# Optimization experiments

Measured on AMD Instinct MI355X. Metric: run time of the kernel, lower is better.

## Reference

```python
import jax, jax.numpy as jnp
import numpy as np

LN_EPS = 1e-5
BN_EPS = 1e-5


def setup_inputs() -> dict:
    key = jax.random.key(0)
    ks = jax.random.split(key, 16)
    b, n = 16, 256
    sc = 0.1
    inp = {
        "x": jax.random.normal(ks[0], (b, n, 4), jnp.float32),
        # proj: Linear(4, 64)
        "proj_w": jax.random.normal(ks[1], (4, 64), jnp.float32) * sc,
        "proj_b": jnp.zeros((64,), jnp.float32),
        # sigma_net: Linear(128,64) -> LayerNorm(64) -> ReLU -> Linear(64,1) -> Softplus
        "s_w1": jax.random.normal(ks[2], (128, 64), jnp.float32) * sc,
        "s_b1": jnp.zeros((64,), jnp.float32),
        "ln_g": jnp.ones((64,), jnp.float32),
        "ln_b": jnp.zeros((64,), jnp.float32),
        "s_w2": jax.random.normal(ks[3], (64, 1), jnp.float32) * sc,
        "s_b2": jnp.zeros((1,), jnp.float32),
        # gnn weight
        "gnn_w": jax.random.normal(ks[4], (64, 64), jnp.float32) * sc,
        # classifier: Linear(128,64) -> BatchNorm1d(64) -> ELU -> Dropout(eval) -> Linear(64,2)
        "c_w1": jax.random.normal(ks[5], (128, 64), jnp.float32) * sc,
        "c_b1": jnp.zeros((64,), jnp.float32),
        "bn_g": jnp.ones((64,), jnp.float32),
        "bn_b": jnp.zeros((64,), jnp.float32),
        "bn_mean": jnp.zeros((64,), jnp.float32),
        "bn_var": jnp.ones((64,), jnp.float32),
        "c_w2": jax.random.normal(ks[6], (64, 2), jnp.float32) * sc,
        "c_b2": jnp.zeros((2,), jnp.float32),
    }
    return inp


def reference(x, proj_w, proj_b, s_w1, s_b1, ln_g, ln_b, s_w2, s_b2,
              gnn_w, c_w1, c_b1, bn_g, bn_b, bn_mean, bn_var, c_w2, c_b2):
    # h: [b, n, 64]
    h = jax.nn.elu(x @ proj_w + proj_b)

    # sigma_net(cat([xi, xj])) == hi @ s_w1[:64] + hj @ s_w1[64:] + s_b1, broadcast pairwise
    a_i = h @ s_w1[:64]            # [b, n, 64]
    a_j = h @ s_w1[64:]            # [b, n, 64]
    pre = a_i[:, :, None, :] + a_j[:, None, :, :] + s_b1  # [b, n, n, 64]
    mu = jnp.mean(pre, axis=-1, keepdims=True)
    var = jnp.mean((pre - mu) ** 2, axis=-1, keepdims=True)
    ln = (pre - mu) * jax.lax.rsqrt(var + LN_EPS) * ln_g + ln_b
    sig_pre = jax.nn.relu(ln) @ s_w2 + s_b2               # [b, n, n, 1]
    sigmas = jax.nn.softplus(sig_pre[..., 0])             # [b, n, n]

    # squared pairwise distance via gram trick: ||hi - hj||^2
    sq = jnp.sum(h * h, axis=-1)                          # [b, n]
    gram = jnp.einsum("bid,bjd->bij", h, h)               # [b, n, n]
    d2 = jnp.maximum(sq[:, :, None] + sq[:, None, :] - 2.0 * gram, 0.0)
    adj = jnp.exp(-d2 / (2.0 * sigmas ** 2 + 1e-6))       # [b, n, n]

    h_agg = jnp.einsum("bij,bjd->bid", adj, h) @ gnn_w    # [b, n, 64]
    h_res = jax.nn.elu(h_agg + h)

    pooled = jnp.concatenate([h_res.mean(axis=1), h_res.max(axis=1)], axis=1)  # [b, 128]

    z = pooled @ c_w1 + c_b1
    z = (z - bn_mean) * jax.lax.rsqrt(bn_var + BN_EPS) * bn_g + bn_b  # BN eval mode
    z = jax.nn.elu(z)                                      # Dropout is identity in eval
    return z @ c_w2 + c_b2                                 # [b, 2]
```

## Files before the change

kernel.cpp:

```cpp
#include <hip/hip_runtime.h>
#include <math.h>

#define OFF_H      0
#define OFF_HT     262144
#define OFF_AI     524288
#define OFF_AJT    786432
#define OFF_SAI    1048576
#define OFF_QAI    1052672
#define OFF_SAJ    1056768
#define OFF_QAJ    1060864
#define OFF_SQH    1064960
#define OFF_HRES   1069056

__device__ __forceinline__ float elu_f(float x) { return x > 0.f ? x : expm1f(x); }

__global__ __launch_bounds__(256) void k1_embed(
    const float* __restrict__ x,
    const float* __restrict__ proj_w, const float* __restrict__ proj_b,
    const float* __restrict__ s_w1, const float* __restrict__ s_b1,
    float* __restrict__ h, float* __restrict__ hT,
    float* __restrict__ a_i, float* __restrict__ a_jT,
    float* __restrict__ sa_i, float* __restrict__ qa_i,
    float* __restrict__ sa_j, float* __restrict__ qa_j,
    float* __restrict__ sqh)
{
    __shared__ float w_sh[8192];
    int tid = threadIdx.x;
    #pragma unroll
    for (int r = 0; r < 8; ++r)
        *(float4*)&w_sh[(r*256 + tid)*4] = *(const float4*)&s_w1[(r*256 + tid)*4];
    __syncthreads();

    int lane = tid & 63;
    int wave = tid >> 6;
    int row0 = blockIdx.x * 8;

    float pw0 = proj_w[lane], pw1 = proj_w[64+lane], pw2 = proj_w[128+lane],
          pw3 = proj_w[192+lane], pb = proj_b[lane], b1 = s_b1[lane];

    #pragma unroll
    for (int r = 0; r < 2; ++r) {
        int row = row0 + wave*2 + r;
        int b = row >> 8, i = row & 255;
        float4 xv = *(const float4*)&x[row*4];
        float hv = elu_f(xv.x*pw0 + xv.y*pw1 + xv.z*pw2 + xv.w*pw3 + pb);

        float ai = b1, aj = 0.f;
        #pragma unroll 8
        for (int e = 0; e < 64; ++e) {
            float he = __shfl(hv, e);
            ai = fmaf(he, w_sh[e*64 + lane], ai);
            aj = fmaf(he, w_sh[(64+e)*64 + lane], aj);
        }
        h[row*64 + lane]   = hv;
        hT[b*64*256 + lane*256 + i] = hv;
        a_i[row*64 + lane] = ai;
        a_jT[b*64*256 + lane*256 + i] = aj;

        float v1 = ai, v2 = ai*ai, v3 = aj, v4 = aj*aj, v5 = hv*hv;
        #pragma unroll
        for (int off = 32; off > 0; off >>= 1) {
            v1 += __shfl_xor(v1, off);
            v2 += __shfl_xor(v2, off);
            v3 += __shfl_xor(v3, off);
            v4 += __shfl_xor(v4, off);
            v5 += __shfl_xor(v5, off);
        }
        if (lane == 0) {
            sa_i[row] = v1; qa_i[row] = v2;
            sa_j[row] = v3; qa_j[row] = v4;
            sqh[row]  = v5;
        }
    }
}

__global__ __launch_bounds__(256) void k2_pair(
    const float* __restrict__ a_i, const float* __restrict__ a_jT,
    const float* __restrict__ h, const float* __restrict__ hT,
    const float* __restrict__ sa_i, const float* __restrict__ qa_i,
    const float* __restrict__ sa_j, const float* __restrict__ qa_j,
    const float* __restrict__ sqh,
    const float* __restrict__ ln_g, const float* __restrict__ ln_b,
    const float* __restrict__ s_w2, const float* __restrict__ s_b2,
    const float* __restrict__ gnn_w,
    float* __restrict__ h_res)
{
    int bi0 = blockIdx.x * 4;
    int b   = bi0 >> 8;
    int j   = threadIdx.x;
    int gj  = b*256 + j;

    __shared__ float aiT[64][4], hiT[64][4];
    __shared__ float gbw[64][4];
    __shared__ float sai_s[4], qai_s[4], sqi_s[4];
    __shared__ float adj_sh[256][4];
    __shared__ float part_sh[4][4][64];
    __shared__ float hagg_sh[4][64];

    {
        int i = j >> 6, d = j & 63;
        aiT[d][i] = a_i[(bi0+i)*64 + d];
        hiT[d][i] = h[(bi0+i)*64 + d];
    }
    if (j < 64) {
        gbw[j][0] = ln_g[j]; gbw[j][1] = ln_b[j]; gbw[j][2] = s_w2[j]; gbw[j][3] = 0.f;
    }
    if (j < 4) {
        sai_s[j] = sa_i[bi0+j]; qai_s[j] = qa_i[bi0+j]; sqi_s[j] = sqh[bi0+j];
    }
    float saj = sa_j[gj], qaj = qa_j[gj], sqj = sqh[gj];
    float b2  = s_b2[0];
    __syncthreads();

    const float* ajb = a_jT + b*64*256;
    const float* htb = hT   + b*64*256;

    float ga[4] = {0.f,0.f,0.f,0.f}, gh[4] = {0.f,0.f,0.f,0.f};
    #pragma unroll 8
    for (int d = 0; d < 64; ++d) {
        float ajd = ajb[d*256 + j];
        float hjd = htb[d*256 + j];
        float4 A = *(const float4*)&aiT[d][0];
        float4 H = *(const float4*)&hiT[d][0];
        ga[0] = fmaf(A.x, ajd, ga[0]); ga[1] = fmaf(A.y, ajd, ga[1]);
        ga[2] = fmaf(A.z, ajd, ga[2]); ga[3] = fmaf(A.w, ajd, ga[3]);
        gh[0] = fmaf(H.x, hjd, gh[0]); gh[1] = fmaf(H.y, hjd, gh[1]);
        gh[2] = fmaf(H.z, hjd, gh[2]); gh[3] = fmaf(H.w, hjd, gh[3]);
    }

    float rs4[4], nr4[4], d24[4];
    #pragma unroll
    for (int i = 0; i < 4; ++i) {
        float mu  = (sai_s[i] + saj) * (1.f/64.f);
        float pss = qai_s[i] + qaj + 2.f*ga[i];
        float var = pss * (1.f/64.f) - mu*mu;
        rs4[i] = rsqrtf(var + 1e-5f);
        nr4[i] = -mu * rs4[i];
        d24[i] = fmaxf(sqi_s[i] + sqj - 2.f*gh[i], 0.f);
    }

    float acc[4] = {0.f,0.f,0.f,0.f};
    #pragma unroll 8
    for (int d = 0; d < 64; ++d) {
        float ajd = ajb[d*256 + j];
        float4 A = *(const float4*)&aiT[d][0];
        float4 G = *(const float4*)&gbw[d][0];
        float t0 = fmaxf(fmaf(fmaf(A.x + ajd, rs4[0], nr4[0]), G.x, G.y), 0.f);
        acc[0] = fmaf(t0, G.z, acc[0]);
        float t1 = fmaxf(fmaf(fmaf(A.y + ajd, rs4[1], nr4[1]), G.x, G.y), 0.f);
        acc[1] = fmaf(t1, G.z, acc[1]);
        float t2 = fmaxf(fmaf(fmaf(A.z + ajd, rs4[2], nr4[2]), G.x, G.y), 0.f);
        acc[2] = fmaf(t2, G.z, acc[2]);
        float t3 = fmaxf(fmaf(fmaf(A.w + ajd, rs4[3], nr4[3]), G.x, G.y), 0.f);
        acc[3] = fmaf(t3, G.z, acc[3]);
    }

    {
        float4 av;
        float sp0 = acc[0] + b2;
        float sg0 = fmaxf(sp0, 0.f) + log1pf(expf(-fabsf(sp0)));
        av.x = expf(-d24[0] / (2.f*sg0*sg0 + 1e-6f));
        float sp1 = acc[1] + b2;
        float sg1 = fmaxf(sp1, 0.f) + log1pf(expf(-fabsf(sp1)));
        av.y = expf(-d24[1] / (2.f*sg1*sg1 + 1e-6f));
        float sp2 = acc[2] + b2;
        float sg2 = fmaxf(sp2, 0.f) + log1pf(expf(-fabsf(sp2)));
        av.z = expf(-d24[2] / (2.f*sg2*sg2 + 1e-6f));
        float sp3 = acc[3] + b2;
        float sg3 = fmaxf(sp3, 0.f) + log1pf(expf(-fabsf(sp3)));
        av.w = expf(-d24[3] / (2.f*sg3*sg3 + 1e-6f));
        *(float4*)&adj_sh[j][0] = av;
    }
    __syncthreads();

    int d = j & 63, q = j >> 6;
    const float* hb = h + b*256*64;
    float part[4] = {0.f,0.f,0.f,0.f};
    #pragma unroll 8
    for (int k = 0; k < 64; ++k) {
        int jj = q*64 + k;
        float hv = hb[jj*64 + d];
        float4 a4 = *(const float4*)&adj_sh[jj][0];
        part[0] = fmaf(a4.x, hv, part[0]);
        part[1] = fmaf(a4.y, hv, part[1]);
        part[2] = fmaf(a4.z, hv, part[2]);
        part[3] = fmaf(a4.w, hv, part[3]);
    }
    #pragma unroll
    for (int i = 0; i < 4; ++i) part_sh[q][i][d] = part[i];
    __syncthreads();

    {
        int i = j >> 6, dd = j & 63;
        hagg_sh[i][dd] = part_sh[0][i][dd] + part_sh[1][i][dd]
                       + part_sh[2][i][dd] + part_sh[3][i][dd];
    }
    __syncthreads();

    {
        int i = j >> 6, lane = j & 63;
        float accg = 0.f;
        #pragma unroll 8
        for (int e = 0; e < 64; ++e)
            accg = fmaf(hagg_sh[i][e], gnn_w[e*64 + lane], accg);
        h_res[(bi0+i)*64 + lane] = elu_f(accg + hiT[lane][i]);
    }
}

__global__ __launch_bounds__(256) void k4_pool_cls(
    const float* __restrict__ h_res,
    const float* __restrict__ c_w1, const float* __restrict__ c_b1,
    const float* __restrict__ bn_g, const float* __restrict__ bn_b,
    const float* __restrict__ bn_mean, const float* __restrict__ bn_var,
    const float* __restrict__ c_w2, const float* __restrict__ c_b2,
    float* __restrict__ out)
{
    int b = blockIdx.x;
    int tid = threadIdx.x;
    int d = tid & 63, q = tid >> 6;
    const float* hb = h_res + b*256*64;

    float sum = 0.f, mx = -INFINITY;
    #pragma unroll 8
    for (int k = 0; k < 64; ++k) {
        float v = hb[(q*64+k)*64 + d];
        sum += v; mx = fmaxf(mx, v);
    }
    __shared__ float sum_sh[256], max_sh[256];
    __shared__ float pm_sh[64], px_sh[64];
    sum_sh[tid] = sum; max_sh[tid] = mx;
    __syncthreads();
    if (tid < 64) {
        float tsum = sum_sh[tid] + sum_sh[64+tid] + sum_sh[128+tid] + sum_sh[192+tid];
        float tmax = fmaxf(fmaxf(max_sh[tid], max_sh[64+tid]),
                           fmaxf(max_sh[128+tid], max_sh[192+tid]));
        pm_sh[tid] = tsum * (1.f/256.f);
        px_sh[tid] = tmax;
    }
    __syncthreads();
    if (tid < 64) {
        float acc = c_b1[tid];
        #pragma unroll
        for (int e = 0; e < 64; ++e) {
            acc += pm_sh[e] * c_w1[e*64 + tid];
            acc += px_sh[e] * c_w1[(64+e)*64 + tid];
        }
        float z = (acc - bn_mean[tid]) * rsqrtf(bn_var[tid] + 1e-5f) * bn_g[tid] + bn_b[tid];
        z = elu_f(z);
        float c0 = z * c_w2[tid*2 + 0];
        float c1 = z * c_w2[tid*2 + 1];
        for (int off = 32; off > 0; off >>= 1) {
            c0 += __shfl_down(c0, off);
            c1 += __shfl_down(c1, off);
        }
        if (tid == 0) {
            out[b*2 + 0] = c0 + c_b2[0];
            out[b*2 + 1] = c1 + c_b2[1];
        }
    }
}

extern "C" void kernel_launch(void* const* d_in, const int* in_sizes, int n_in,
                              void* d_out, int out_size, void* d_ws, size_t ws_size,
                              hipStream_t stream) {
    const float* x       = (const float*)d_in[0];
    const float* proj_w  = (const float*)d_in[1];
    const float* proj_b  = (const float*)d_in[2];
    const float* s_w1    = (const float*)d_in[3];
    const float* s_b1    = (const float*)d_in[4];
    const float* ln_g    = (const float*)d_in[5];
    const float* ln_b    = (const float*)d_in[6];
    const float* s_w2    = (const float*)d_in[7];
    const float* s_b2    = (const float*)d_in[8];
    const float* gnn_w   = (const float*)d_in[9];
    const float* c_w1    = (const float*)d_in[10];
    const float* c_b1    = (const float*)d_in[11];
    const float* bn_g    = (const float*)d_in[12];
    const float* bn_b    = (const float*)d_in[13];
    const float* bn_mean = (const float*)d_in[14];
    const float* bn_var  = (const float*)d_in[15];
    const float* c_w2    = (const float*)d_in[16];
    const float* c_b2    = (const float*)d_in[17];

    float* w = (float*)d_ws;
    float* h     = w + OFF_H;
    float* hT    = w + OFF_HT;
    float* a_i   = w + OFF_AI;
    float* a_jT  = w + OFF_AJT;
    float* sa_i  = w + OFF_SAI;
    float* qa_i  = w + OFF_QAI;
    float* sa_j  = w + OFF_SAJ;
    float* qa_j  = w + OFF_QAJ;
    float* sqh   = w + OFF_SQH;
    float* h_res = w + OFF_HRES;
    float* out   = (float*)d_out;

    k1_embed<<<512, 256, 0, stream>>>(x, proj_w, proj_b, s_w1, s_b1,
                                      h, hT, a_i, a_jT,
                                      sa_i, qa_i, sa_j, qa_j, sqh);
    k2_pair<<<1024, 256, 0, stream>>>(a_i, a_jT, h, hT,
                                      sa_i, qa_i, sa_j, qa_j, sqh,
                                      ln_g, ln_b, s_w2, s_b2, gnn_w, h_res);
    k4_pool_cls<<<16, 256, 0, stream>>>(h_res, c_w1, c_b1, bn_g, bn_b,
                                        bn_mean, bn_var, c_w2, c_b2, out);
}
```

Before: 49.48 us.

## Compute pairwise Gram matrices with bf16 MFMA in a separate kernel

```diff
diff --git a/kernel.cpp b/kernel.cpp
--- a/kernel.cpp
+++ b/kernel.cpp
@@ -2,24 +2,35 @@
 #include <math.h>
 
 #define OFF_H      0
-#define OFF_HT     262144
-#define OFF_AI     524288
-#define OFF_AJT    786432
-#define OFF_SAI    1048576
-#define OFF_QAI    1052672
-#define OFF_SAJ    1056768
-#define OFF_QAJ    1060864
-#define OFF_SQH    1064960
-#define OFF_HRES   1069056
+#define OFF_AI     262144
+#define OFF_AJT    524288
+#define OFF_SAI    786432
+#define OFF_QAI    790528
+#define OFF_SAJ    794624
+#define OFF_QAJ    798720
+#define OFF_SQH    802816
+#define OFF_GA     806912
+#define OFF_GH     1855488
+#define OFF_HRES   2904064
+#define OFF_BF     3166208
+
+typedef __attribute__((ext_vector_type(8))) short bf16x8;
+typedef __attribute__((ext_vector_type(4))) float f32x4;
 
 __device__ __forceinline__ float elu_f(float x) { return x > 0.f ? x : expm1f(x); }
+
+__device__ __forceinline__ short f2bf(float f) {
+    unsigned u = __float_as_uint(f);
+    unsigned r = (u + 0x7FFF + ((u >> 16) & 1)) >> 16;
+    return (short)r;
+}
 
 __global__ __launch_bounds__(256) void k1_embed(
     const float* __restrict__ x,
     const float* __restrict__ proj_w, const float* __restrict__ proj_b,
     const float* __restrict__ s_w1, const float* __restrict__ s_b1,
-    float* __restrict__ h, float* __restrict__ hT,
-    float* __restrict__ a_i, float* __restrict__ a_jT,
+    float* __restrict__ h, float* __restrict__ a_i, float* __restrict__ a_jT,
+    short* __restrict__ ai_bf, short* __restrict__ aj_bf, short* __restrict__ h_bf,
     float* __restrict__ sa_i, float* __restrict__ qa_i,
     float* __restrict__ sa_j, float* __restrict__ qa_j,
     float* __restrict__ sqh)
@@ -53,9 +64,11 @@
             aj = fmaf(he, w_sh[(64+e)*64 + lane], aj);
         }
         h[row*64 + lane]   = hv;
-        hT[b*64*256 + lane*256 + i] = hv;
         a_i[row*64 + lane] = ai;
         a_jT[b*64*256 + lane*256 + i] = aj;
+        ai_bf[row*64 + lane] = f2bf(ai);
+        aj_bf[row*64 + lane] = f2bf(aj);
+        h_bf [row*64 + lane] = f2bf(hv);
 
         float v1 = ai, v2 = ai*ai, v3 = aj, v4 = aj*aj, v5 = hv*hv;
         #pragma unroll
@@ -74,9 +87,41 @@
     }
 }
 
+__global__ __launch_bounds__(64) void kgram(
+    const short* __restrict__ ai_bf, const short* __restrict__ aj_bf,
+    const short* __restrict__ h_bf,
+    float* __restrict__ ga, float* __restrict__ gh)
+{
+    int bid = blockIdx.x;
+    int g = bid & 1;
+    int s = (bid >> 1) & 15;
+    int b = bid >> 5;
+    const short* XA = (g ? h_bf : ai_bf) + b*256*64;
+    const short* XB = (g ? h_bf : aj_bf) + b*256*64;
+    float* G = (g ? gh : ga) + (b*256 + s*16)*256;
+
+    int l = threadIdx.x, lo = l & 15, hi = l >> 4;
+
+    bf16x8 a0 = *(const bf16x8*)&XA[(s*16 + lo)*64 + hi*8];
+    bf16x8 a1 = *(const bf16x8*)&XA[(s*16 + lo)*64 + 32 + hi*8];
+
+    #pragma unroll 4
+    for (int jt = 0; jt < 16; ++jt) {
+        bf16x8 b0 = *(const bf16x8*)&XB[(jt*16 + lo)*64 + hi*8];
+        bf16x8 b1 = *(const bf16x8*)&XB[(jt*16 + lo)*64 + 32 + hi*8];
+        f32x4 c = {0.f, 0.f, 0.f, 0.f};
+        c = __builtin_amdgcn_mfma_f32_16x16x32_bf16(a0, b0, c, 0, 0, 0);
+        c = __builtin_amdgcn_mfma_f32_16x16x32_bf16(a1, b1, c, 0, 0, 0);
+        #pragma unroll
+        for (int r = 0; r < 4; ++r)
+            G[(hi*4 + r)*256 + jt*16 + lo] = c[r];
+    }
+}
+
 __global__ __launch_bounds__(256) void k2_pair(
     const float* __restrict__ a_i, const float* __restrict__ a_jT,
-    const float* __restrict__ h, const float* __restrict__ hT,
+    const float* __restrict__ h,
+    const float* __restrict__ ga_m, const float* __restrict__ gh_m,
     const float* __restrict__ sa_i, const float* __restrict__ qa_i,
     const float* __restrict__ sa_j, const float* __restrict__ qa_j,
     const float* __restrict__ sqh,
@@ -110,23 +155,14 @@
     }
     float saj = sa_j[gj], qaj = qa_j[gj], sqj = sqh[gj];
     float b2  = s_b2[0];
-    __syncthreads();
-
-    const float* ajb = a_jT + b*64*256;
-    const float* htb = hT   + b*64*256;
-
-    float ga[4] = {0.f,0.f,0.f,0.f}, gh[4] = {0.f,0.f,0.f,0.f};
-    #pragma unroll 8
-    for (int d = 0; d < 64; ++d) {
-        float ajd = ajb[d*256 + j];
-        float hjd = htb[d*256 + j];
-        float4 A = *(const float4*)&aiT[d][0];
-        float4 H = *(const float4*)&hiT[d][0];
-        ga[0] = fmaf(A.x, ajd, ga[0]); ga[1] = fmaf(A.y, ajd, ga[1]);
-        ga[2] = fmaf(A.z, ajd, ga[2]); ga[3] = fmaf(A.w, ajd, ga[3]);
-        gh[0] = fmaf(H.x, hjd, gh[0]); gh[1] = fmaf(H.y, hjd, gh[1]);
-        gh[2] = fmaf(H.z, hjd, gh[2]); gh[3] = fmaf(H.w, hjd, gh[3]);
-    }
+
+    float ga[4], gh[4];
+    #pragma unroll
+    for (int i = 0; i < 4; ++i) {
+        ga[i] = ga_m[(bi0+i)*256 + j];
+        gh[i] = gh_m[(bi0+i)*256 + j];
+    }
+    __syncthreads();
 
     float rs4[4], nr4[4], d24[4];
     #pragma unroll
@@ -139,6 +175,7 @@
         d24[i] = fmaxf(sqi_s[i] + sqj - 2.f*gh[i], 0.f);
     }
 
+    const float* ajb = a_jT + b*64*256;
     float acc[4] = {0.f,0.f,0.f,0.f};
     #pragma unroll 8
     for (int d = 0; d < 64; ++d) {
@@ -284,7 +321,6 @@
 
     float* w = (float*)d_ws;
     float* h     = w + OFF_H;
-    float* hT    = w + OFF_HT;
     float* a_i   = w + OFF_AI;
     float* a_jT  = w + OFF_AJT;
     float* sa_i  = w + OFF_SAI;
@@ -292,13 +328,19 @@
     float* sa_j  = w + OFF_SAJ;
     float* qa_j  = w + OFF_QAJ;
     float* sqh   = w + OFF_SQH;
+    float* ga    = w + OFF_GA;
+    float* gh    = w + OFF_GH;
     float* h_res = w + OFF_HRES;
+    short* ai_bf = (short*)(w + OFF_BF);
+    short* aj_bf = ai_bf + 262144;
+    short* h_bf  = ai_bf + 524288;
     float* out   = (float*)d_out;
 
     k1_embed<<<512, 256, 0, stream>>>(x, proj_w, proj_b, s_w1, s_b1,
-                                      h, hT, a_i, a_jT,
+                                      h, a_i, a_jT, ai_bf, aj_bf, h_bf,
                                       sa_i, qa_i, sa_j, qa_j, sqh);
-    k2_pair<<<1024, 256, 0, stream>>>(a_i, a_jT, h, hT,
+    kgram<<<512, 64, 0, stream>>>(ai_bf, aj_bf, h_bf, ga, gh);
+    k2_pair<<<1024, 256, 0, stream>>>(a_i, a_jT, h, ga, gh,
                                       sa_i, qa_i, sa_j, qa_j, sqh,
                                       ln_g, ln_b, s_w2, s_b2, gnn_w, h_res);
     k4_pool_cls<<<16, 256, 0, stream>>>(h_res, c_w1, c_b1, bn_g, bn_b,
```

New measurement: 52.24 us. 1.06x slower.

## Interleave a_j and h into float2 layout and vectorize adjacency aggregation

Applied to the files above, without the earlier changes.

```diff
diff --git a/kernel.cpp b/kernel.cpp
--- a/kernel.cpp
+++ b/kernel.cpp
@@ -2,9 +2,8 @@
 #include <math.h>
 
 #define OFF_H      0
-#define OFF_HT     262144
-#define OFF_AI     524288
-#define OFF_AJT    786432
+#define OFF_AI     262144
+#define OFF_AJH    524288
 #define OFF_SAI    1048576
 #define OFF_QAI    1052672
 #define OFF_SAJ    1056768
@@ -18,8 +17,7 @@
     const float* __restrict__ x,
     const float* __restrict__ proj_w, const float* __restrict__ proj_b,
     const float* __restrict__ s_w1, const float* __restrict__ s_b1,
-    float* __restrict__ h, float* __restrict__ hT,
-    float* __restrict__ a_i, float* __restrict__ a_jT,
+    float* __restrict__ h, float* __restrict__ a_i, float2* __restrict__ ajh,
     float* __restrict__ sa_i, float* __restrict__ qa_i,
     float* __restrict__ sa_j, float* __restrict__ qa_j,
     float* __restrict__ sqh)
@@ -53,9 +51,8 @@
             aj = fmaf(he, w_sh[(64+e)*64 + lane], aj);
         }
         h[row*64 + lane]   = hv;
-        hT[b*64*256 + lane*256 + i] = hv;
         a_i[row*64 + lane] = ai;
-        a_jT[b*64*256 + lane*256 + i] = aj;
+        ajh[b*16384 + lane*256 + i] = make_float2(aj, hv);
 
         float v1 = ai, v2 = ai*ai, v3 = aj, v4 = aj*aj, v5 = hv*hv;
         #pragma unroll
@@ -75,8 +72,8 @@
 }
 
 __global__ __launch_bounds__(256) void k2_pair(
-    const float* __restrict__ a_i, const float* __restrict__ a_jT,
-    const float* __restrict__ h, const float* __restrict__ hT,
+    const float* __restrict__ a_i, const float2* __restrict__ ajh,
+    const float* __restrict__ h,
     const float* __restrict__ sa_i, const float* __restrict__ qa_i,
     const float* __restrict__ sa_j, const float* __restrict__ qa_j,
     const float* __restrict__ sqh,
@@ -94,7 +91,7 @@
     __shared__ float gbw[64][4];
     __shared__ float sai_s[4], qai_s[4], sqi_s[4];
     __shared__ float adj_sh[256][4];
-    __shared__ float part_sh[4][4][64];
+    __shared__ float pool[16*4*64];
     __shared__ float hagg_sh[4][64];
 
     {
@@ -112,20 +109,18 @@
     float b2  = s_b2[0];
     __syncthreads();
 
-    const float* ajb = a_jT + b*64*256;
-    const float* htb = hT   + b*64*256;
+    const float2* ajhb = ajh + b*16384;
 
     float ga[4] = {0.f,0.f,0.f,0.f}, gh[4] = {0.f,0.f,0.f,0.f};
     #pragma unroll 8
     for (int d = 0; d < 64; ++d) {
-        float ajd = ajb[d*256 + j];
-        float hjd = htb[d*256 + j];
+        float2 v = ajhb[d*256 + j];
         float4 A = *(const float4*)&aiT[d][0];
         float4 H = *(const float4*)&hiT[d][0];
-        ga[0] = fmaf(A.x, ajd, ga[0]); ga[1] = fmaf(A.y, ajd, ga[1]);
-        ga[2] = fmaf(A.z, ajd, ga[2]); ga[3] = fmaf(A.w, ajd, ga[3]);
-        gh[0] = fmaf(H.x, hjd, gh[0]); gh[1] = fmaf(H.y, hjd, gh[1]);
-        gh[2] = fmaf(H.z, hjd, gh[2]); gh[3] = fmaf(H.w, hjd, gh[3]);
+        ga[0] = fmaf(A.x, v.x, ga[0]); ga[1] = fmaf(A.y, v.x, ga[1]);
+        ga[2] = fmaf(A.z, v.x, ga[2]); ga[3] = fmaf(A.w, v.x, ga[3]);
+        gh[0] = fmaf(H.x, v.y, gh[0]); gh[1] = fmaf(H.y, v.y, gh[1]);
+        gh[2] = fmaf(H.z, v.y, gh[2]); gh[3] = fmaf(H.w, v.y, gh[3]);
     }
 
     float rs4[4], nr4[4], d24[4];
@@ -142,7 +137,7 @@
     float acc[4] = {0.f,0.f,0.f,0.f};
     #pragma unroll 8
     for (int d = 0; d < 64; ++d) {
-        float ajd = ajb[d*256 + j];
+        float ajd = ajhb[d*256 + j].x;
         float4 A = *(const float4*)&aiT[d][0];
         float4 G = *(const float4*)&gbw[d][0];
         float t0 = fmaxf(fmaf(fmaf(A.x + ajd, rs4[0], nr4[0]), G.x, G.y), 0.f);
@@ -173,27 +168,38 @@
     }
     __syncthreads();
 
-    int d = j & 63, q = j >> 6;
-    const float* hb = h + b*256*64;
-    float part[4] = {0.f,0.f,0.f,0.f};
-    #pragma unroll 8
-    for (int k = 0; k < 64; ++k) {
-        int jj = q*64 + k;
-        float hv = hb[jj*64 + d];
-        float4 a4 = *(const float4*)&adj_sh[jj][0];
-        part[0] = fmaf(a4.x, hv, part[0]);
-        part[1] = fmaf(a4.y, hv, part[1]);
-        part[2] = fmaf(a4.z, hv, part[2]);
-        part[3] = fmaf(a4.w, hv, part[3]);
-    }
-    #pragma unroll
-    for (int i = 0; i < 4; ++i) part_sh[q][i][d] = part[i];
-    __syncthreads();
-
-    {
-        int i = j >> 6, dd = j & 63;
-        hagg_sh[i][dd] = part_sh[0][i][dd] + part_sh[1][i][dd]
-                       + part_sh[2][i][dd] + part_sh[3][i][dd];
+    {
+        int q = j >> 4, dq = j & 15;
+        const float* hb = h + b*256*64;
+        float4 p0 = {0.f,0.f,0.f,0.f}, p1 = p0, p2 = p0, p3 = p0;
+        #pragma unroll
+        for (int k = 0; k < 16; ++k) {
+            int jj = q*16 + k;
+            float4 hv = *(const float4*)&hb[jj*64 + dq*4];
+            float4 a4 = *(const float4*)&adj_sh[jj][0];
+            p0.x=fmaf(a4.x,hv.x,p0.x); p0.y=fmaf(a4.x,hv.y,p0.y);
+            p0.z=fmaf(a4.x,hv.z,p0.z); p0.w=fmaf(a4.x,hv.w,p0.w);
+            p1.x=fmaf(a4.y,hv.x,p1.x); p1.y=fmaf(a4.y,hv.y,p1.y);
+            p1.z=fmaf(a4.y,hv.z,p1.z); p1.w=fmaf(a4.y,hv.w,p1.w);
+            p2.x=fmaf(a4.z,hv.x,p2.x); p2.y=fmaf(a4.z,hv.y,p2.y);
+            p2.z=fmaf(a4.z,hv.z,p2.z); p2.w=fmaf(a4.z,hv.w,p2.w);
+            p3.x=fmaf(a4.w,hv.x,p3.x); p3.y=fmaf(a4.w,hv.y,p3.y);
+            p3.z=fmaf(a4.w,hv.z,p3.z); p3.w=fmaf(a4.w,hv.w,p3.w);
+        }
+        *(float4*)&pool[(q*4 + 0)*64 + dq*4] = p0;
+        *(float4*)&pool[(q*4 + 1)*64 + dq*4] = p1;
+        *(float4*)&pool[(q*4 + 2)*64 + dq*4] = p2;
+        *(float4*)&pool[(q*4 + 3)*64 + dq*4] = p3;
+    }
+    __syncthreads();
+
+    {
+        int i = j >> 6, d = j & 63;
+        float s = 0.f;
+        #pragma unroll
+        for (int q2 = 0; q2 < 16; ++q2)
+            s += pool[(q2*4 + i)*64 + d];
+        hagg_sh[i][d] = s;
     }
     __syncthreads();
 
@@ -283,22 +289,21 @@
     const float* c_b2    = (const float*)d_in[17];
 
     float* w = (float*)d_ws;
-    float* h     = w + OFF_H;
-    float* hT    = w + OFF_HT;
-    float* a_i   = w + OFF_AI;
-    float* a_jT  = w + OFF_AJT;
-    float* sa_i  = w + OFF_SAI;
-    float* qa_i  = w + OFF_QAI;
-    float* sa_j  = w + OFF_SAJ;
-    float* qa_j  = w + OFF_QAJ;
-    float* sqh   = w + OFF_SQH;
-    float* h_res = w + OFF_HRES;
-    float* out   = (float*)d_out;
+    float*  h     = w + OFF_H;
+    float*  a_i   = w + OFF_AI;
+    float2* ajh   = (float2*)(w + OFF_AJH);
+    float*  sa_i  = w + OFF_SAI;
+    float*  qa_i  = w + OFF_QAI;
+    float*  sa_j  = w + OFF_SAJ;
+    float*  qa_j  = w + OFF_QAJ;
+    float*  sqh   = w + OFF_SQH;
+    float*  h_res = w + OFF_HRES;
+    float*  out   = (float*)d_out;
 
     k1_embed<<<512, 256, 0, stream>>>(x, proj_w, proj_b, s_w1, s_b1,
-                                      h, hT, a_i, a_jT,
+                                      h, a_i, ajh,
                                       sa_i, qa_i, sa_j, qa_j, sqh);
-    k2_pair<<<1024, 256, 0, stream>>>(a_i, a_jT, h, hT,
+    k2_pair<<<1024, 256, 0, stream>>>(a_i, ajh, h,
                                       sa_i, qa_i, sa_j, qa_j, sqh,
                                       ln_g, ln_b, s_w2, s_b2, gnn_w, h_res);
     k4_pool_cls<<<16, 256, 0, stream>>>(h_res, c_w1, c_b1, bn_g, bn_b,
```

New measurement: 49.68 us. No clear change (+0.4%).
